# Kernel tuning notes

Hardware: AMD Instinct MI355X
Metric: run time of the kernel (lower is better)

The kernel has to match this reference:

```python
import jax, jax.numpy as jnp
import numpy as np

N_NODES = 50000
N_EDGES = 800000
D_FEAT = 128      # node feature dim
D_IN = 2 * D_FEAT # MLP input (concat of x_i and x_j - x_i)
D_OUT = 256


def setup_inputs() -> dict:
    key = jax.random.key(0)
    ks = jax.random.split(key, 8)
    x = jax.random.normal(ks[0], (N_NODES, D_FEAT), dtype=jnp.float32)
    edge_index = jax.random.randint(ks[1], (2, N_EDGES), 0, N_NODES, dtype=jnp.int64)
    s1 = 1.0 / np.sqrt(D_IN)
    s2 = 1.0 / np.sqrt(D_OUT)
    W1 = jax.random.uniform(ks[2], (D_IN, D_OUT), jnp.float32, -s1, s1)
    b1 = jax.random.uniform(ks[3], (D_OUT,), jnp.float32, -s1, s1)
    W2 = jax.random.uniform(ks[4], (D_OUT, D_OUT), jnp.float32, -s2, s2)
    b2 = jax.random.uniform(ks[5], (D_OUT,), jnp.float32, -s2, s2)
    W3 = jax.random.uniform(ks[6], (D_OUT, D_OUT), jnp.float32, -s2, s2)
    b3 = jax.random.uniform(ks[7], (D_OUT,), jnp.float32, -s2, s2)
    return {"x": x, "edge_index": edge_index, "W1": W1, "b1": b1,
            "W2": W2, "b2": b2, "W3": W3, "b3": b3}


def reference(x, edge_index, W1, b1, W2, b2, W3, b3):
    # EdgeConv: for edge (j -> i): msg = MLP(concat([x_i, x_j - x_i])); max-aggregate at i
    src, dst = edge_index[0], edge_index[1]
    x_i = x[dst]                       # [E, D_FEAT] target features
    x_j = x[src]                       # [E, D_FEAT] source features
    e = jnp.concatenate([x_i, x_j - x_i], axis=-1)  # [E, 2*D_FEAT]
    h = jax.nn.relu(e @ W1 + b1)
    h = jax.nn.relu(h @ W2 + b2)
    h = h @ W3 + b3                    # [E, D_OUT]
    out = jax.ops.segment_max(h, dst, num_segments=N_NODES)  # [N, D_OUT]
    # nodes with no incoming edges -> 0 (PyG scatter-max fill)
    return jnp.where(jnp.isfinite(out), out, jnp.zeros((), out.dtype))
```

## Files before the change

kernel.cpp:

```cpp
#include <hip/hip_runtime.h>
#include <stdint.h>


#define N_NODES 50000
#define N_EDGES 800000
#define EPB 64
#define NBLK 12500

typedef __attribute__((ext_vector_type(4))) float f32x4;
typedef __attribute__((ext_vector_type(8))) _Float16 f16x8;
typedef __attribute__((ext_vector_type(4))) unsigned int u32x4;
typedef __attribute__((ext_vector_type(2))) unsigned int u32x2;

__device__ __forceinline__ unsigned int pkrtz(float a, float b){
  auto p = __builtin_amdgcn_cvt_pkrtz(a, b);
  return __builtin_bit_cast(unsigned int, p);
}
__device__ __forceinline__ unsigned int f16bits(float f){
  _Float16 h = (_Float16)f;
  return (unsigned int)__builtin_bit_cast(unsigned short, h);
}
__device__ __forceinline__ unsigned int pkadd_relu(unsigned int a, unsigned int b){
  unsigned int s, r;
  asm("v_pk_add_f16 %0, %1, %2" : "=v"(s) : "v"(a), "v"(b));
  asm("v_pk_max_f16 %0, %1, %2" : "=v"(r) : "v"(s), "v"(0u));
  return r;
}
__device__ __forceinline__ unsigned int fmap(float f){
  unsigned int u = __builtin_bit_cast(unsigned int, f);
  return (u & 0x80000000u) ? ~u : (u | 0x80000000u);
}
__device__ __forceinline__ bool is64(const unsigned int* e){
  return (e[1] | e[3] | e[5] | e[7] | e[9] | e[11] | e[13] | e[15]) == 0u;
}

extern "C" __global__ void k_hist(const void* __restrict__ eidx, unsigned int* __restrict__ cnt){
  int i = blockIdx.x * 256 + threadIdx.x;
  int d = is64((const unsigned int*)eidx)
        ? (int)((const long long*)eidx)[N_EDGES + i]
        : ((const int*)eidx)[N_EDGES + i];
  atomicAdd(&cnt[d], 1u);
}

extern "C" __global__ void k_psum(const unsigned int* __restrict__ cnt, unsigned int* __restrict__ bsum){
  __shared__ unsigned int red[4];
  const int b = blockIdx.x, t = threadIdx.x, i = b * 256 + t;
  unsigned int v = (i < N_NODES) ? cnt[i] : 0u;
  #pragma unroll
  for (int d = 32; d; d >>= 1) v += __shfl_down(v, d, 64);
  if ((t & 63) == 0) red[t >> 6] = v;
  __syncthreads();
  if (t == 0) bsum[b] = red[0] + red[1] + red[2] + red[3];
}
extern "C" __global__ void __launch_bounds__(256) k_bscan(const unsigned int* __restrict__ bsum,
                                                          unsigned int* __restrict__ bbase){
  __shared__ unsigned int s[256];
  const int t = threadIdx.x;
  unsigned int v = (t < 196) ? bsum[t] : 0u;
  s[t] = v; __syncthreads();
  for (int d = 1; d < 256; d <<= 1){
    unsigned int u = (t >= d) ? s[t - d] : 0u;
    __syncthreads(); s[t] += u; __syncthreads();
  }
  if (t < 196) bbase[t] = s[t] - v;
}
extern "C" __global__ void k_apply(const unsigned int* __restrict__ cnt,
                                   const unsigned int* __restrict__ bbase,
                                   unsigned int* __restrict__ off){
  __shared__ unsigned int s[256];
  const int b = blockIdx.x, t = threadIdx.x, i = b * 256 + t;
  unsigned int v = (i < N_NODES) ? cnt[i] : 0u;
  s[t] = v; __syncthreads();
  for (int d = 1; d < 256; d <<= 1){
    unsigned int u = (t >= d) ? s[t - d] : 0u;
    __syncthreads(); s[t] += u; __syncthreads();
  }
  if (i < N_NODES) off[i] = bbase[b] + s[t] - v;
}

extern "C" __global__ void k_bucket(const void* __restrict__ eidx,
                                    unsigned int* __restrict__ cur, unsigned int* __restrict__ sPair){
  int i = blockIdx.x * 256 + threadIdx.x;
  int s, d;
  if (is64((const unsigned int*)eidx)){
    const long long* p = (const long long*)eidx;
    s = (int)p[i]; d = (int)p[N_EDGES + i];
  } else {
    const int* p = (const int*)eidx;
    s = p[i]; d = p[N_EDGES + i];
  }
  unsigned int pos = atomicAdd(&cur[d], 1u);
  sPair[pos] = (unsigned int)s | ((unsigned int)d << 16);
}

extern "C" __global__ void k_wprep(const float* __restrict__ W1, const float* __restrict__ W2,
                                   const float* __restrict__ W3,
                                   unsigned short* __restrict__ w2s, unsigned short* __restrict__ w3s,
                                   unsigned short* __restrict__ wdf){
  int t = blockIdx.x * 256 + threadIdx.x;
  if (t < 16384){
    const float* W = (t & 8192) ? W3 : W2;
    unsigned short* o = (t & 8192) ? w3s : w2s;
    int r = t & 8191, lane = r & 63, blk = r >> 6;
    int m  = (blk >> 3) * 16 + (lane & 15);
    int k0 = (blk & 7) * 32 + (lane >> 4) * 8;
    u32x4 ov;
    #pragma unroll
    for (int j = 0; j < 4; j++){
      unsigned int lo = f16bits(W[(size_t)(k0 + 2*j    ) * 256 + m]);
      unsigned int hi = f16bits(W[(size_t)(k0 + 2*j + 1) * 256 + m]);
      ov[j] = lo | (hi << 16);
    }
    *(u32x4*)(o + (size_t)r * 8) = ov;
  } else {
    int r = t - 16384, lane = r & 63, blk = r >> 6;
    int m  = (blk >> 2) * 16 + (lane & 15);
    int k0 = (blk & 3) * 32 + (lane >> 4) * 8;
    u32x4 ov;
    #pragma unroll
    for (int j = 0; j < 4; j++){
      float vlo, vhi;
      int ka = k0 + 2*j, kb = k0 + 2*j + 1;
      if (m < 256){
        vlo = W1[(size_t)ka * 256 + m] - W1[(size_t)(ka + 128) * 256 + m];
        vhi = W1[(size_t)kb * 256 + m] - W1[(size_t)(kb + 128) * 256 + m];
      } else {
        vlo = W1[(size_t)(ka + 128) * 256 + (m - 256)];
        vhi = W1[(size_t)(kb + 128) * 256 + (m - 256)];
      }
      ov[j] = f16bits(vlo) | (f16bits(vhi) << 16);
    }
    *(u32x4*)(wdf + (size_t)r * 8) = ov;
  }
}

extern "C" __global__ void __launch_bounds__(256) k_acm(
    const float* __restrict__ x, const unsigned short* __restrict__ wdf,
    const float* __restrict__ b1, unsigned short* __restrict__ acb){
  __shared__ unsigned char smx[16384];
  const int tid = threadIdx.x, lane = tid & 63, w = tid >> 6;
  const int n0 = blockIdx.x * 64;
  {
    const int nl = tid >> 2, q = tid & 3;
    int node = n0 + nl; if (node > N_NODES - 1) node = N_NODES - 1;
    const f32x4* xp = (const f32x4*)(x + (size_t)node * 128 + q * 32);
    unsigned char* base = smx + (((nl >> 4) * 256 + q * 64 + (nl & 15)) << 4);
    #pragma unroll
    for (int s = 0; s < 4; s++){
      f32x4 v0 = xp[s * 2], v1 = xp[s * 2 + 1];
      u32x4 ov = { pkrtz(v0[0], v0[1]), pkrtz(v0[2], v0[3]),
                   pkrtz(v1[0], v1[1]), pkrtz(v1[2], v1[3]) };
      *(u32x4*)(base + s * 256) = ov;
    }
  }
  __syncthreads();
  const int lm = lane & 15, g = lane >> 4;
  f32x4 acc[8][4];
  #pragma unroll
  for (int mf = 0; mf < 8; mf++)
    #pragma unroll
    for (int nf = 0; nf < 4; nf++) acc[mf][nf] = (f32x4){0.f, 0.f, 0.f, 0.f};
  #pragma unroll
  for (int ks = 0; ks < 4; ks++){
    f16x8 af[8], bfr[4];
    #pragma unroll
    for (int mf = 0; mf < 8; mf++)
      af[mf] = __builtin_bit_cast(f16x8, *(const u32x4*)(wdf + (size_t)(((w * 8 + mf) * 4 + ks) * 64 + lane) * 8));
    #pragma unroll
    for (int nf = 0; nf < 4; nf++)
      bfr[nf] = __builtin_bit_cast(f16x8, *(const u32x4*)(smx + nf * 4096 + ks * 1024 + lane * 16));
    #pragma unroll
    for (int mf = 0; mf < 8; mf++)
      #pragma unroll
      for (int nf = 0; nf < 4; nf++)
        acc[mf][nf] = __builtin_amdgcn_mfma_f32_16x16x32_f16(af[mf], bfr[nf], acc[mf][nf], 0, 0, 0);
  }
  #pragma unroll
  for (int mf = 0; mf < 8; mf++){
    const int m0 = w * 128 + mf * 16 + g * 4;
    f32x4 bb = (f32x4){0.f, 0.f, 0.f, 0.f};
    if (w < 2) bb = *(const f32x4*)(b1 + m0);
    #pragma unroll
    for (int nf = 0; nf < 4; nf++){
      int node = n0 + nf * 16 + lm;
      if (node < N_NODES){
        u32x2 pv = { pkrtz(acc[mf][nf][0] + bb[0], acc[mf][nf][1] + bb[1]),
                     pkrtz(acc[mf][nf][2] + bb[2], acc[mf][nf][3] + bb[3]) };
        *(u32x2*)(acb + (size_t)node * 512 + m0) = pv;
      }
    }
  }
}

extern "C" __global__ void __launch_bounds__(256, 4) k_edge(
    const unsigned short* __restrict__ acb,
    const unsigned short* __restrict__ w2f, const unsigned short* __restrict__ w3f,
    const float* __restrict__ b2, const float* __restrict__ b3,
    const unsigned int* __restrict__ sPair,
    unsigned int* __restrict__ outu){
  __shared__ unsigned char sm[32768];
  __shared__ int dstI[EPB];
  __shared__ int srcI[EPB];
  const int tid = threadIdx.x;
  const int lane = tid & 63;
  const int w = tid >> 6;

  const int bid = blockIdx.x;
  const int xcd = bid & 7, idx = bid >> 3;
  const int sb = (xcd < 4) ? xcd * 1563 : 4 * 1563 + (xcd - 4) * 1562;
  const int e0 = (sb + idx) * EPB;

  f16x8 afp[4];
  #pragma unroll
  for (int mf = 0; mf < 4; mf++)
    afp[mf] = __builtin_bit_cast(f16x8, *(const u32x4*)(w2f + (size_t)(((w * 4 + mf) * 8 + 0) * 64 + lane) * 8));

  if (tid < EPB){
    unsigned int pr = sPair[e0 + tid];
    srcI[tid] = (int)(pr & 0xFFFFu);
    dstI[tid] = (int)(pr >> 16);
  }
  __syncthreads();

  {
    const int e = tid >> 2, q = tid & 3;
    const unsigned short* pa = acb + (size_t)dstI[e] * 512 + q * 64;
    const unsigned short* pc = acb + (size_t)srcI[e] * 512 + 256 + q * 64;
    unsigned char* base = sm + (e >> 4) * 8192 + (e & 15) * 16;
    #pragma unroll
    for (int j = 0; j < 8; j++){
      u32x4 ua = *(const u32x4*)(pa + j * 8);
      u32x4 uc = *(const u32x4*)(pc + j * 8);
      u32x4 ov;
      #pragma unroll
      for (int t2 = 0; t2 < 4; t2++) ov[t2] = pkadd_relu(ua[t2], uc[t2]);
      *(u32x4*)(base + (q * 2 + (j >> 2)) * 1024 + (j & 3) * 256) = ov;
    }
  }
  __syncthreads();

  const int lm = lane & 15, g = lane >> 4;
  f32x4 acc[4][4];
  {
    #pragma unroll
    for (int mf = 0; mf < 4; mf++){
      const f32x4 bb = *(const f32x4*)(b2 + w * 64 + mf * 16 + g * 4);
      #pragma unroll
      for (int nf = 0; nf < 4; nf++) acc[mf][nf] = bb;
    }
  }

  #pragma unroll
  for (int ks = 0; ks < 8; ks++){
    f16x8 af[4], bfr[4];
    #pragma unroll
    for (int mf = 0; mf < 4; mf++)
      af[mf] = (ks == 0) ? afp[mf]
             : __builtin_bit_cast(f16x8, *(const u32x4*)(w2f + (size_t)(((w * 4 + mf) * 8 + ks) * 64 + lane) * 8));
    #pragma unroll
    for (int nf = 0; nf < 4; nf++)
      bfr[nf] = __builtin_bit_cast(f16x8, *(const u32x4*)(sm + nf * 8192 + ks * 1024 + lane * 16));
    __builtin_amdgcn_s_setprio(1);
    #pragma unroll
    for (int mf = 0; mf < 4; mf++)
      #pragma unroll
      for (int nf = 0; nf < 4; nf++)
        acc[mf][nf] = __builtin_amdgcn_mfma_f32_16x16x32_f16(af[mf], bfr[nf], acc[mf][nf], 0, 0, 0);
    __builtin_amdgcn_s_setprio(0);
  }

  #pragma unroll
  for (int mf = 0; mf < 4; mf++)
    afp[mf] = __builtin_bit_cast(f16x8, *(const u32x4*)(w3f + (size_t)(((w * 4 + mf) * 8 + 0) * 64 + lane) * 8));
  __syncthreads();

  {
    #pragma unroll
    for (int mf = 0; mf < 4; mf++){
      const int m0 = w * 64 + mf * 16 + g * 4;
      const int boff = (m0 >> 5) * 1024 + ((m0 >> 3) & 3) * 256 + lm * 16 + (m0 & 7) * 2;
      #pragma unroll
      for (int nf = 0; nf < 4; nf++){
        float v0 = fmaxf(acc[mf][nf][0], 0.f);
        float v1 = fmaxf(acc[mf][nf][1], 0.f);
        float v2 = fmaxf(acc[mf][nf][2], 0.f);
        float v3 = fmaxf(acc[mf][nf][3], 0.f);
        u32x2 pv = { pkrtz(v0, v1), pkrtz(v2, v3) };
        *(u32x2*)(sm + nf * 8192 + boff) = pv;
      }
    }
  }
  __syncthreads();

  {
    #pragma unroll
    for (int mf = 0; mf < 4; mf++){
      const f32x4 bb = *(const f32x4*)(b3 + w * 64 + mf * 16 + g * 4);
      #pragma unroll
      for (int nf = 0; nf < 4; nf++) acc[mf][nf] = bb;
    }
  }
  #pragma unroll
  for (int ks = 0; ks < 8; ks++){
    f16x8 af[4], bfr[4];
    #pragma unroll
    for (int mf = 0; mf < 4; mf++)
      af[mf] = (ks == 0) ? afp[mf]
             : __builtin_bit_cast(f16x8, *(const u32x4*)(w3f + (size_t)(((w * 4 + mf) * 8 + ks) * 64 + lane) * 8));
    #pragma unroll
    for (int nf = 0; nf < 4; nf++)
      bfr[nf] = __builtin_bit_cast(f16x8, *(const u32x4*)(sm + nf * 8192 + ks * 1024 + lane * 16));
    __builtin_amdgcn_s_setprio(1);
    #pragma unroll
    for (int mf = 0; mf < 4; mf++)
      #pragma unroll
      for (int nf = 0; nf < 4; nf++)
        acc[mf][nf] = __builtin_amdgcn_mfma_f32_16x16x32_f16(af[mf], bfr[nf], acc[mf][nf], 0, 0, 0);
    __builtin_amdgcn_s_setprio(0);
  }
  __syncthreads();

  float vmaxf = -__builtin_inff();
  int curDst = dstI[0];
  const int t4 = tid * 4;
  #pragma unroll
  for (int half = 0; half < 2; half++){
    #pragma unroll
    for (int mf = 0; mf < 4; mf++){
      const int m0 = w * 64 + mf * 16 + g * 4;
      #pragma unroll
      for (int nfl = 0; nfl < 2; nfl++){
        const int r = nfl * 16 + lm;
        const int nf = half * 2 + nfl;
        *(f32x4*)(sm + r * 1024 + ((m0 * 4) ^ ((r & 7) << 4))) = acc[mf][nf];
      }
    }
    __syncthreads();
    for (int it = 0; it < 32; it++){
      float v = *(const float*)(sm + it * 1024 + (t4 ^ ((it & 7) << 4)));
      const int d = dstI[half * 32 + it];
      if (d != curDst){
        atomicMax(outu + (size_t)curDst * 256 + tid, fmap(vmaxf));
        curDst = d; vmaxf = -__builtin_inff();
      }
      vmaxf = fmaxf(vmaxf, v);
    }
    __syncthreads();
  }
  atomicMax(outu + (size_t)curDst * 256 + tid, fmap(vmaxf));
}

extern "C" __global__ void k_fix(u32x4* __restrict__ o){
  size_t i = (size_t)blockIdx.x * 256 + threadIdx.x;
  u32x4 u = o[i];
  #pragma unroll
  for (int j = 0; j < 4; j++)
    u[j] = (u[j] == 0u) ? 0u : ((u[j] & 0x80000000u) ? (u[j] ^ 0x80000000u) : ~u[j]);
  o[i] = u;
}

extern "C" void kernel_launch(void* const* d_in, const int* in_sizes, int n_in,
                              void* d_out, int out_size, void* d_ws, size_t ws_size,
                              hipStream_t stream){
  const float* x  = (const float*)d_in[0];
  const void*  ei = d_in[1];
  const float* W1 = (const float*)d_in[2];
  const float* b1 = (const float*)d_in[3];
  const float* W2 = (const float*)d_in[4];
  const float* b2 = (const float*)d_in[5];
  const float* W3 = (const float*)d_in[6];
  const float* b3 = (const float*)d_in[7];

  const size_t AC_BYTES = (size_t)N_NODES * 512 * 2;
  const size_t W_BYTES  = 256 * 256 * 2;
  const size_t P_BYTES  = (size_t)N_EDGES * 4;
  const size_t C_BYTES  = 200704;
  char* ws = (char*)d_ws;
  size_t o = 0;
  unsigned short* acb  = (unsigned short*)(ws + o); o += AC_BYTES;
  unsigned short* w2s  = (unsigned short*)(ws + o); o += W_BYTES;
  unsigned short* w3s  = (unsigned short*)(ws + o); o += W_BYTES;
  unsigned short* wdf  = (unsigned short*)(ws + o); o += W_BYTES;
  unsigned int*  sPair = (unsigned int*)(ws + o);   o += P_BYTES;
  unsigned int*  cnt   = (unsigned int*)(ws + o);   o += C_BYTES;
  unsigned int*  offA  = (unsigned int*)(ws + o);   o += C_BYTES;
  unsigned int*  bsum  = (unsigned int*)(ws + o);   o += 1024;
  unsigned int*  bbase = (unsigned int*)(ws + o);   o += 1024;
  if (ws_size < o) return;

  (void)hipMemsetAsync(cnt, 0, C_BYTES, stream);
  k_hist<<<N_EDGES / 256, 256, 0, stream>>>(ei, cnt);
  k_psum<<<196, 256, 0, stream>>>(cnt, bsum);
  k_bscan<<<1, 256, 0, stream>>>(bsum, bbase);
  k_apply<<<196, 256, 0, stream>>>(cnt, bbase, offA);
  k_bucket<<<N_EDGES / 256, 256, 0, stream>>>(ei, offA, sPair);
  k_wprep<<<96, 256, 0, stream>>>(W1, W2, W3, w2s, w3s, wdf);
  k_acm<<<(N_NODES + 63) / 64, 256, 0, stream>>>(x, wdf, b1, acb);
  (void)hipMemsetAsync(d_out, 0, (size_t)out_size * 4, stream);
  k_edge<<<NBLK, 256, 0, stream>>>(acb, w2s, w3s, b2, b3, sPair, (unsigned int*)d_out);
  k_fix<<<out_size / 1024, 256, 0, stream>>>((u32x4*)d_out);
}
```

Measured before the change: 438.3 us.

## Stage MLP outputs as packed fp16 and split segment-max across two row streams

The final-layer accumulators are converted to packed fp16 (round-toward-zero) before being written to shared memory, so all 64 edge rows fit in one pass instead of two halves with extra barriers. Each thread now handles two adjacent output columns over every other edge row, taking the max with packed fp16 instructions before converting back to float for the global atomicMax. This removes one store/sync round and halves the shared-memory traffic, but it rounds the outputs to fp16 and doubles the number of atomic calls per flush, since each thread flushes two columns and the edge rows are split between two threads.

```diff
diff --git a/kernel.cpp b/kernel.cpp
--- a/kernel.cpp
+++ b/kernel.cpp
@@ -25,6 +25,17 @@
   asm("v_pk_add_f16 %0, %1, %2" : "=v"(s) : "v"(a), "v"(b));
   asm("v_pk_max_f16 %0, %1, %2" : "=v"(r) : "v"(s), "v"(0u));
   return r;
+}
+__device__ __forceinline__ unsigned int pkmax(unsigned int a, unsigned int b){
+  unsigned int r;
+  asm("v_pk_max_f16 %0, %1, %2" : "=v"(r) : "v"(a), "v"(b));
+  return r;
+}
+__device__ __forceinline__ float f16lo2f(unsigned int v){
+  return (float)__builtin_bit_cast(_Float16, (unsigned short)(v & 0xFFFFu));
+}
+__device__ __forceinline__ float f16hi2f(unsigned int v){
+  return (float)__builtin_bit_cast(_Float16, (unsigned short)(v >> 16));
 }
 __device__ __forceinline__ unsigned int fmap(float f){
   unsigned int u = __builtin_bit_cast(unsigned int, f);
@@ -320,34 +331,41 @@
   }
   __syncthreads();
 
-  float vmaxf = -__builtin_inff();
-  int curDst = dstI[0];
-  const int t4 = tid * 4;
-  #pragma unroll
-  for (int half = 0; half < 2; half++){
+  {
     #pragma unroll
     for (int mf = 0; mf < 4; mf++){
       const int m0 = w * 64 + mf * 16 + g * 4;
       #pragma unroll
-      for (int nfl = 0; nfl < 2; nfl++){
-        const int r = nfl * 16 + lm;
-        const int nf = half * 2 + nfl;
-        *(f32x4*)(sm + r * 1024 + ((m0 * 4) ^ ((r & 7) << 4))) = acc[mf][nf];
+      for (int nf = 0; nf < 4; nf++){
+        const int r = nf * 16 + lm;
+        u32x2 pv = { pkrtz(acc[mf][nf][0], acc[mf][nf][1]),
+                     pkrtz(acc[mf][nf][2], acc[mf][nf][3]) };
+        *(u32x2*)(sm + r * 512 + ((m0 * 2) ^ ((r & 7) << 4))) = pv;
       }
     }
-    __syncthreads();
-    for (int it = 0; it < 32; it++){
-      float v = *(const float*)(sm + it * 1024 + (t4 ^ ((it & 7) << 4)));
-      const int d = dstI[half * 32 + it];
+  }
+  __syncthreads();
+
+  {
+    const int p = tid & 127, sub = tid >> 7;
+    unsigned int vmax = 0xFC00FC00u;
+    int curDst = dstI[sub];
+    for (int k = 0; k < 32; k++){
+      const int rl = 2 * k + sub;
+      unsigned int v = *(const unsigned int*)(sm + rl * 512 + ((p * 4) ^ ((rl & 7) << 4)));
+      const int d = dstI[rl];
       if (d != curDst){
-        atomicMax(outu + (size_t)curDst * 256 + tid, fmap(vmaxf));
-        curDst = d; vmaxf = -__builtin_inff();
+        unsigned int* o = outu + (size_t)curDst * 256 + 2 * p;
+        atomicMax(o,     fmap(f16lo2f(vmax)));
+        atomicMax(o + 1, fmap(f16hi2f(vmax)));
+        curDst = d; vmax = 0xFC00FC00u;
       }
-      vmaxf = fmaxf(vmaxf, v);
-    }
-    __syncthreads();
-  }
-  atomicMax(outu + (size_t)curDst * 256 + tid, fmap(vmaxf));
+      vmax = pkmax(vmax, v);
+    }
+    unsigned int* o = outu + (size_t)curDst * 256 + 2 * p;
+    atomicMax(o,     fmap(f16lo2f(vmax)));
+    atomicMax(o + 1, fmap(f16hi2f(vmax)));
+  }
 }
 
 extern "C" __global__ void k_fix(u32x4* __restrict__ o){
```

Measured after the change: 450.0 us. 1.03x slower.
